# Optimization experiments

Hardware: AMD Instinct MI355X
Metric: run time of the kernel (lower is better)

The kernel has to match this reference:

```python
import jax, jax.numpy as jnp
import numpy as np

NHID = 512
T_K, T_Q, B = 256, 128, 8


def setup_inputs() -> dict:
    key = jax.random.key(0)
    k1, k2, k3, k4, k5 = jax.random.split(key, 5)
    query = jax.random.normal(k1, (T_Q, B, NHID), dtype=jnp.float32)
    c_key = jax.random.normal(k2, (T_K, B, NHID), dtype=jnp.float32)
    mask = jax.random.randint(k3, (T_K, B), 0, 2).astype(bool)
    # att_mlp params: Linear(2*nhid, nhid) -> Tanh -> Linear(nhid, 1)
    # stored as [in, out] so y = x @ W + b (torch Linear weight transposed)
    W1 = jax.random.normal(k4, (2 * NHID, NHID), dtype=jnp.float32) / np.sqrt(2 * NHID)
    b1 = jnp.zeros((NHID,), dtype=jnp.float32)
    W2 = jax.random.normal(k5, (NHID, 1), dtype=jnp.float32) / np.sqrt(NHID)
    b2 = jnp.zeros((1,), dtype=jnp.float32)
    return {"query": query, "c_key": c_key, "mask": mask,
            "W1": W1, "b1": b1, "W2": W2, "b2": b2}


def reference(query, c_key, mask, W1, b1, W2, b2):
    H = query.shape[-1]
    # cat([k_expand, q_expand], -1) @ W1 == k @ W1[:H] + q @ W1[H:]
    # (avoids materializing the [T_k, T_q, B, 2H] concat the torch code builds)
    k_proj = jnp.einsum('kbh,hd->kbd', c_key, W1[:H])   # [T_k, B, H]
    q_proj = jnp.einsum('qbh,hd->qbd', query, W1[H:])   # [T_q, B, H]
    h = jnp.tanh(k_proj[:, None, :, :] + q_proj[None, :, :, :] + b1)  # [T_k, T_q, B, H]
    att_score = jnp.einsum('kqbh,ho->kqb', h, W2) + b2[0]             # [T_k, T_q, B]
    att_score = jnp.where(mask[:, None, :], -jnp.inf, att_score)
    att_prob = jax.nn.softmax(att_score, axis=0)                      # softmax over keys
    # c_val defaults to c_key in the original forward
    ant_vec = jnp.einsum('kqb,kbh->qbh', att_prob, c_key)             # [T_q, B, H]
    return ant_vec, att_prob
```

## Files before the change

### kernel.cpp

```cpp
#include <hip/hip_runtime.h>
#include <math.h>

#define NHID 512
#define T_K  256
#define T_Q  128
#define BB   8

constexpr float C2L2E = 2.8853900817779268f;
constexpr float L2E   = 1.4426950408889634f;

__device__ __forceinline__ float fexp2(float x) { return __builtin_amdgcn_exp2f(x); }
__device__ __forceinline__ float frcp(float x)  { return __builtin_amdgcn_rcpf(x); }

typedef __attribute__((ext_vector_type(8))) short bf16x8;
typedef __attribute__((ext_vector_type(4))) float f32x4;

__device__ __forceinline__ unsigned short f2bf(float x) {
    unsigned u = __builtin_bit_cast(unsigned, x);
    unsigned r = (u + 0x7FFFu + ((u >> 16) & 1u)) >> 16;
    return (unsigned short)r;
}
__device__ __forceinline__ float bf2f(unsigned short h) {
    unsigned u = ((unsigned)h) << 16;
    return __builtin_bit_cast(float, u);
}
__device__ __forceinline__ unsigned packbf(float a, float b) {
    return (unsigned)f2bf(a) | ((unsigned)f2bf(b) << 16);
}

__global__ __launch_bounds__(256) void convert_kernel(
    const float* __restrict__ W1, const float* __restrict__ ckey,
    unsigned short* __restrict__ bt_hi, unsigned short* __restrict__ bt_lo,
    unsigned int* __restrict__ ckp)
{
    const int bid = blockIdx.x;
    const int t   = threadIdx.x;
    if (bid < 128) {
        const int kt = bid & 15;
        const int nt = bid >> 4;
        __shared__ float tile[64][65];
        const int r  = t >> 2;
        const int c0 = (t & 3) * 16;
        const float* src = W1 + (size_t)(kt * 64 + r) * 512 + nt * 64 + c0;
        #pragma unroll
        for (int j = 0; j < 4; ++j) {
            const float4 v = *(const float4*)&src[j * 4];
            tile[r][c0 + j * 4 + 0] = v.x; tile[r][c0 + j * 4 + 1] = v.y;
            tile[r][c0 + j * 4 + 2] = v.z; tile[r][c0 + j * 4 + 3] = v.w;
        }
        __syncthreads();
        const size_t dst = (size_t)((kt >> 3) * 512 + nt * 64 + r) * 512
                         + (size_t)((kt & 7) * 64 + c0);
        #pragma unroll
        for (int j4 = 0; j4 < 4; ++j4) {
            ushort4 h, l;
            #pragma unroll
            for (int e = 0; e < 4; ++e) {
                const float x = tile[c0 + j4 * 4 + e][r];
                const unsigned short hb = f2bf(x);
                ((unsigned short*)&h)[e] = hb;
                ((unsigned short*)&l)[e] = f2bf(x - bf2f(hb));
            }
            *(ushort4*)&bt_hi[dst + j4 * 4] = h;
            *(ushort4*)&bt_lo[dst + j4 * 4] = l;
        }
    } else {
        const int cb = bid - 128;
        const int b  = cb >> 5;
        const int kt = cb & 31;
        const int kloc = t >> 5;
        const int g    = t & 31;
        const int k = kt * 8 + kloc;
        const float* src = ckey + ((size_t)k * 8 + b) * 512 + g * 16;
        const float4 v0 = *(const float4*)&src[0];
        const float4 v1 = *(const float4*)&src[4];
        const float4 v2 = *(const float4*)&src[8];
        const float4 v3 = *(const float4*)&src[12];
        uint4 o0, o1;
        o0.x = packbf(v0.x, v0.y); o0.y = packbf(v0.z, v0.w);
        o0.z = packbf(v1.x, v1.y); o0.w = packbf(v1.z, v1.w);
        o1.x = packbf(v2.x, v2.y); o1.y = packbf(v2.z, v2.w);
        o1.z = packbf(v3.x, v3.y); o1.w = packbf(v3.z, v3.w);
        unsigned int* dst = ckp + ((size_t)b * 256 + k) * 256 + g * 8;
        *(uint4*)&dst[0] = o0;
        *(uint4*)&dst[4] = o1;
    }
}

__global__ __launch_bounds__(256) void proj_kernel(
    const float* __restrict__ qry, const float* __restrict__ ckey,
    const unsigned short* __restrict__ bt_hi, const unsigned short* __restrict__ bt_lo,
    const float* __restrict__ b1,
    uint2* __restrict__ ektq, float* __restrict__ eq)
{
    const int row0 = blockIdx.x * 64;
    const int col0 = blockIdx.y * 64;
    const bool isK = row0 < 2048;
    const int bhalf = isK ? 0 : 512;

    __shared__ __align__(16) unsigned short As_h[64 * 64];
    __shared__ __align__(16) unsigned short As_l[64 * 64];
    __shared__ __align__(16) unsigned short Bs_h[64 * 64];
    __shared__ __align__(16) unsigned short Bs_l[64 * 64];

    const int t    = threadIdx.x;
    const int wave = t >> 6;
    const int lane = t & 63;
    const int wm = (wave & 1) * 32;
    const int wn = (wave >> 1) * 32;

    f32x4 acc[2][2] = {};

    const int sr = t >> 2;
    const int sc = (t & 3) * 16;
    const float* gA = (isK ? ckey + (size_t)(row0 + sr) * 512
                           : qry  + (size_t)(row0 - 2048 + sr) * 512) + sc;
    const unsigned short* gBh = bt_hi + (size_t)(bhalf + col0 + sr) * 512 + sc;
    const unsigned short* gBl = bt_lo + (size_t)(bhalf + col0 + sr) * 512 + sc;
    const int c0c = sc >> 3;
    const int sw0 = ((c0c + 0) ^ (sr & 7)) * 8;
    const int sw1 = ((c0c + 1) ^ (sr & 7)) * 8;

    const int quad = lane >> 4, fr = lane & 15;

    float4 pa0 = *(const float4*)&gA[0];
    float4 pa1 = *(const float4*)&gA[4];
    float4 pa2 = *(const float4*)&gA[8];
    float4 pa3 = *(const float4*)&gA[12];
    uint4  pbh0 = *(const uint4*)&gBh[0], pbh1 = *(const uint4*)&gBh[8];
    uint4  pbl0 = *(const uint4*)&gBl[0], pbl1 = *(const uint4*)&gBl[8];

    for (int k0 = 0; k0 < 512; k0 += 64) {
        float fa[16];
        *(float4*)&fa[0] = pa0; *(float4*)&fa[4] = pa1;
        *(float4*)&fa[8] = pa2; *(float4*)&fa[12] = pa3;
        union { uint4 v; unsigned short s[8]; } h0, l0, h1, l1;
        #pragma unroll
        for (int e = 0; e < 8; ++e) {
            const unsigned short hb = f2bf(fa[e]);
            h0.s[e] = hb; l0.s[e] = f2bf(fa[e] - bf2f(hb));
        }
        #pragma unroll
        for (int e = 0; e < 8; ++e) {
            const unsigned short hb = f2bf(fa[8 + e]);
            h1.s[e] = hb; l1.s[e] = f2bf(fa[8 + e] - bf2f(hb));
        }
        __syncthreads();
        *(uint4*)&As_h[sr * 64 + sw0] = h0.v; *(uint4*)&As_h[sr * 64 + sw1] = h1.v;
        *(uint4*)&As_l[sr * 64 + sw0] = l0.v; *(uint4*)&As_l[sr * 64 + sw1] = l1.v;
        *(uint4*)&Bs_h[sr * 64 + sw0] = pbh0; *(uint4*)&Bs_h[sr * 64 + sw1] = pbh1;
        *(uint4*)&Bs_l[sr * 64 + sw0] = pbl0; *(uint4*)&Bs_l[sr * 64 + sw1] = pbl1;
        __syncthreads();

        if (k0 + 64 < 512) {
            pa0 = *(const float4*)&gA[k0 + 64];
            pa1 = *(const float4*)&gA[k0 + 68];
            pa2 = *(const float4*)&gA[k0 + 72];
            pa3 = *(const float4*)&gA[k0 + 76];
            pbh0 = *(const uint4*)&gBh[k0 + 64]; pbh1 = *(const uint4*)&gBh[k0 + 72];
            pbl0 = *(const uint4*)&gBl[k0 + 64]; pbl1 = *(const uint4*)&gBl[k0 + 72];
        }

        #pragma unroll
        for (int ks = 0; ks < 2; ++ks) {
            const int cchunk = ks * 4 + quad;
            bf16x8 afh[2], afl[2], bfh[2], bfl[2];
            #pragma unroll
            for (int mt = 0; mt < 2; ++mt) {
                const int m = wm + mt * 16 + fr;
                afh[mt] = *(const bf16x8*)&As_h[m * 64 + ((cchunk ^ (m & 7)) * 8)];
                afl[mt] = *(const bf16x8*)&As_l[m * 64 + ((cchunk ^ (m & 7)) * 8)];
            }
            #pragma unroll
            for (int nt = 0; nt < 2; ++nt) {
                const int n = wn + nt * 16 + fr;
                bfh[nt] = *(const bf16x8*)&Bs_h[n * 64 + ((cchunk ^ (n & 7)) * 8)];
                bfl[nt] = *(const bf16x8*)&Bs_l[n * 64 + ((cchunk ^ (n & 7)) * 8)];
            }
            #pragma unroll
            for (int mt = 0; mt < 2; ++mt)
                #pragma unroll
                for (int nt = 0; nt < 2; ++nt) {
                    acc[mt][nt] = __builtin_amdgcn_mfma_f32_16x16x32_bf16(afh[mt], bfh[nt], acc[mt][nt], 0, 0, 0);
                    acc[mt][nt] = __builtin_amdgcn_mfma_f32_16x16x32_bf16(afh[mt], bfl[nt], acc[mt][nt], 0, 0, 0);
                    acc[mt][nt] = __builtin_amdgcn_mfma_f32_16x16x32_bf16(afl[mt], bfh[nt], acc[mt][nt], 0, 0, 0);
                }
        }
    }

    #pragma unroll
    for (int nt = 0; nt < 2; ++nt) {
        const int colg = col0 + wn + nt * 16 + fr;
        const float b1v = b1[colg];
        #pragma unroll
        for (int mt = 0; mt < 2; ++mt) {
            #pragma unroll
            for (int i = 0; i < 4; ++i) {
                const int rowg = row0 + wm + mt * 16 + quad * 4 + i;
                const float v = acc[mt][nt][i];
                if (isK) {
                    const float e = fexp2((v + b1v) * C2L2E);
                    const float ep = __shfl_xor(e, 1, 64);
                    unsigned pk = packbf(e, ep);
                    pk = ((fr & 1) == 0) ? pk
                       : (unsigned)f2bf(ep) | ((unsigned)f2bf(e) << 16);
                    const unsigned pk2 = __shfl_xor(pk, 2, 64);
                    if ((fr & 3) == 0) {
                        const int kidx = rowg >> 3;
                        const int bb   = rowg & 7;
                        const int hq   = colg >> 2;
                        ektq[((size_t)bb * 128 + hq) * 256 + kidx] =
                            make_uint2(pk, pk2);
                    }
                } else {
                    eq[(size_t)(rowg - 2048) * 512 + colg] = fexp2(v * C2L2E);
                }
            }
        }
    }
}

__global__ __launch_bounds__(512) void scoreav_kernel(
    const uint2* __restrict__ ektq, const float* __restrict__ eq,
    const float* __restrict__ W2, const float* __restrict__ b2,
    const int* __restrict__ mask, const unsigned int* __restrict__ ckp,
    float* __restrict__ prob_out, float* __restrict__ out_ant)
{
    const int t    = threadIdx.x;
    const int lane = t & 63;
    const int wave = __builtin_amdgcn_readfirstlane(t >> 6);
    const int kk   = t & 255;
    const int half = t >> 8;
    const int q0   = blockIdx.x * 2;
    const int b    = blockIdx.y;

    __shared__ float eq0s[512], eq1s[512], w2s[512];
    __shared__ float rp[2][512];
    __shared__ float ps[2][256];
    __shared__ float pacc[8][2][512];

    eq0s[t] = eq[((size_t)q0 * 8 + b) * 512 + t];
    eq1s[t] = eq[((size_t)(q0 + 1) * 8 + b) * 512 + t];
    w2s[t]  = W2[t];

    const float4 wA = *(const float4*)&W2[lane * 4];
    const float4 wB = *(const float4*)&W2[256 + lane * 4];
    float s2 = wA.x + wA.y + wA.z + wA.w + wB.x + wB.y + wB.z + wB.w;
    #pragma unroll
    for (int m = 32; m; m >>= 1) s2 += __shfl_xor(s2, m, 64);
    const float base = s2 + b2[0];
    __syncthreads();

    const uint2* __restrict__ ekb = ektq + (size_t)b * 128 * 256 + kk;
    float racc0 = 0.0f, racc1 = 0.0f;

    for (int g = 0; g < 8; ++g) {
        uint2 L[8];
        #pragma unroll
        for (int j = 0; j < 8; ++j)
            L[j] = ekb[(size_t)(half * 64 + g * 8 + j) * 256];
        #pragma unroll
        for (int j = 0; j < 8; ++j) {
            const int h = (half * 64 + g * 8 + j) * 4;
            const float ek0 = __builtin_bit_cast(float, L[j].x << 16);
            const float ek1 = __builtin_bit_cast(float, L[j].x & 0xFFFF0000u);
            const float ek2 = __builtin_bit_cast(float, L[j].y << 16);
            const float ek3 = __builtin_bit_cast(float, L[j].y & 0xFFFF0000u);
            const float4 w  = *(const float4*)&w2s[h];
            const float4 e0 = *(const float4*)&eq0s[h];
            const float4 e1 = *(const float4*)&eq1s[h];
            {
                const float a0 = fmaf(ek0, e0.x, 1.0f);
                const float a1 = fmaf(ek1, e0.y, 1.0f);
                const float a2 = fmaf(ek2, e0.z, 1.0f);
                const float a3 = fmaf(ek3, e0.w, 1.0f);
                const float d01 = a0 * a1, d23 = a2 * a3;
                const float n01 = fmaf(w.x, a1, w.y * a0);
                const float n23 = fmaf(w.z, a3, w.w * a2);
                const float N = fmaf(n01, d23, n23 * d01);
                racc0 = fmaf(N, frcp(d01 * d23), racc0);
            }
            {
                const float a0 = fmaf(ek0, e1.x, 1.0f);
                const float a1 = fmaf(ek1, e1.y, 1.0f);
                const float a2 = fmaf(ek2, e1.z, 1.0f);
                const float a3 = fmaf(ek3, e1.w, 1.0f);
                const float d01 = a0 * a1, d23 = a2 * a3;
                const float n01 = fmaf(w.x, a1, w.y * a0);
                const float n23 = fmaf(w.z, a3, w.w * a2);
                const float N = fmaf(n01, d23, n23 * d01);
                racc1 = fmaf(N, frcp(d01 * d23), racc1);
            }
        }
    }
    rp[0][t] = racc0;
    rp[1][t] = racc1;
    __syncthreads();

    if (t < 256) {
        const int msk = mask[t * 8 + b];
        float s0 = base - 2.0f * (rp[0][t] + rp[0][t + 256]);
        float s1 = base - 2.0f * (rp[1][t] + rp[1][t + 256]);
        if (msk) { s0 = -INFINITY; s1 = -INFINITY; }
        ps[0][t] = s0;
        ps[1][t] = s1;
    }
    __syncthreads();

    if (wave < 2) {
        float4 sv = *(const float4*)&ps[wave][lane * 4];
        float m = fmaxf(fmaxf(sv.x, sv.y), fmaxf(sv.z, sv.w));
        #pragma unroll
        for (int d = 32; d; d >>= 1) m = fmaxf(m, __shfl_xor(m, d, 64));
        float4 pv;
        pv.x = fexp2((sv.x - m) * L2E);
        pv.y = fexp2((sv.y - m) * L2E);
        pv.z = fexp2((sv.z - m) * L2E);
        pv.w = fexp2((sv.w - m) * L2E);
        float sum = pv.x + pv.y + pv.z + pv.w;
        #pragma unroll
        for (int d = 32; d; d >>= 1) sum += __shfl_xor(sum, d, 64);
        const float inv = frcp(sum);
        pv.x *= inv; pv.y *= inv; pv.z *= inv; pv.w *= inv;
        *(float4*)&ps[wave][lane * 4] = pv;
        const int qb_idx = (q0 + wave) * 8 + b;
        const int kbase = lane * 4;
        prob_out[(size_t)(kbase + 0) * 1024 + qb_idx] = pv.x;
        prob_out[(size_t)(kbase + 1) * 1024 + qb_idx] = pv.y;
        prob_out[(size_t)(kbase + 2) * 1024 + qb_idx] = pv.z;
        prob_out[(size_t)(kbase + 3) * 1024 + qb_idx] = pv.w;
    }
    __syncthreads();

    {
        const int h0 = lane * 8;
        float4 aL0 = {}, aH0 = {}, aL1 = {}, aH1 = {};
        const int kstart = wave * 32;
        #pragma unroll 4
        for (int ki = 0; ki < 32; ++ki) {
            const int k = kstart + ki;
            const uint4 U = *(const uint4*)&ckp[((size_t)b * 256 + k) * 256 + lane * 4];
            float4 c0, c1;
            c0.x = __builtin_bit_cast(float, U.x << 16);
            c0.y = __builtin_bit_cast(float, U.x & 0xFFFF0000u);
            c0.z = __builtin_bit_cast(float, U.y << 16);
            c0.w = __builtin_bit_cast(float, U.y & 0xFFFF0000u);
            c1.x = __builtin_bit_cast(float, U.z << 16);
            c1.y = __builtin_bit_cast(float, U.z & 0xFFFF0000u);
            c1.z = __builtin_bit_cast(float, U.w << 16);
            c1.w = __builtin_bit_cast(float, U.w & 0xFFFF0000u);
            const float p0 = ps[0][k];
            const float p1 = ps[1][k];
            aL0.x = fmaf(p0, c0.x, aL0.x); aL0.y = fmaf(p0, c0.y, aL0.y);
            aL0.z = fmaf(p0, c0.z, aL0.z); aL0.w = fmaf(p0, c0.w, aL0.w);
            aH0.x = fmaf(p0, c1.x, aH0.x); aH0.y = fmaf(p0, c1.y, aH0.y);
            aH0.z = fmaf(p0, c1.z, aH0.z); aH0.w = fmaf(p0, c1.w, aH0.w);
            aL1.x = fmaf(p1, c0.x, aL1.x); aL1.y = fmaf(p1, c0.y, aL1.y);
            aL1.z = fmaf(p1, c0.z, aL1.z); aL1.w = fmaf(p1, c0.w, aL1.w);
            aH1.x = fmaf(p1, c1.x, aH1.x); aH1.y = fmaf(p1, c1.y, aH1.y);
            aH1.z = fmaf(p1, c1.z, aH1.z); aH1.w = fmaf(p1, c1.w, aH1.w);
        }
        *(float4*)&pacc[wave][0][h0 + 0] = aL0;
        *(float4*)&pacc[wave][0][h0 + 4] = aH0;
        *(float4*)&pacc[wave][1][h0 + 0] = aL1;
        *(float4*)&pacc[wave][1][h0 + 4] = aH1;
    }
    __syncthreads();

    {
        #pragma unroll
        for (int qi = 0; qi < 2; ++qi) {
            float s = 0.f;
            #pragma unroll
            for (int w = 0; w < 8; ++w) s += pacc[w][qi][t];
            out_ant[((size_t)(q0 + qi) * 8 + b) * 512 + t] = s;
        }
    }
}

extern "C" void kernel_launch(void* const* d_in, const int* in_sizes, int n_in,
                              void* d_out, int out_size, void* d_ws, size_t ws_size,
                              hipStream_t stream)
{
    const float* qry  = (const float*)d_in[0];
    const float* ckey = (const float*)d_in[1];
    const int*   mask = (const int*)d_in[2];
    const float* W1   = (const float*)d_in[3];
    const float* b1   = (const float*)d_in[4];
    const float* W2   = (const float*)d_in[5];
    const float* b2   = (const float*)d_in[6];

    float* out_ant  = (float*)d_out;
    float* out_prob = (float*)d_out + T_Q * BB * NHID;

    float* ws = (float*)d_ws;
    uint2* ws_ektq = (uint2*)ws;
    float* ws_eq  = ws + 524288;
    unsigned short* bt_hi = (unsigned short*)(ws + 1048576);
    unsigned short* bt_lo = (unsigned short*)(ws + 1310720);
    unsigned int* ws_ckp  = (unsigned int*)(ws + 1572864);

    convert_kernel<<<dim3(384), 256, 0, stream>>>(W1, ckey, bt_hi, bt_lo, ws_ckp);
    proj_kernel<<<dim3(48, 8), 256, 0, stream>>>(qry, ckey, bt_hi, bt_lo, b1, ws_ektq, ws_eq);
    scoreav_kernel<<<dim3(64, 8), 512, 0, stream>>>(ws_ektq, ws_eq, W2, b2, mask, ws_ckp,
                                                    out_prob, out_ant);
}
```

Measured before the change: 113.3 us.

## Halve proj_kernel row tile and double-buffer ektq loads in scoreav

The projection GEMM tile shrinks from 64 to 32 rows, doubling the grid from 384 to 768 blocks so more CUs are busy for this small GEMM. Each wave now computes one M-tile instead of two. Separately, the score kernel software-pipelines its loads of the exp(k) data, prefetching the next group of eight rows while the current group is computed. The costs are lower B-tile reuse per block in the GEMM and higher register pressure in the score kernel.

Result: no change. 112.3 us (-0.9%).

```diff
diff --git a/kernel.cpp b/kernel.cpp
--- a/kernel.cpp
+++ b/kernel.cpp
@@ -93,70 +93,64 @@
     const float* __restrict__ b1,
     uint2* __restrict__ ektq, float* __restrict__ eq)
 {
-    const int row0 = blockIdx.x * 64;
+    const int row0 = blockIdx.x * 32;
     const int col0 = blockIdx.y * 64;
     const bool isK = row0 < 2048;
     const int bhalf = isK ? 0 : 512;
 
-    __shared__ __align__(16) unsigned short As_h[64 * 64];
-    __shared__ __align__(16) unsigned short As_l[64 * 64];
+    __shared__ __align__(16) unsigned short As_h[32 * 64];
+    __shared__ __align__(16) unsigned short As_l[32 * 64];
     __shared__ __align__(16) unsigned short Bs_h[64 * 64];
     __shared__ __align__(16) unsigned short Bs_l[64 * 64];
 
     const int t    = threadIdx.x;
     const int wave = t >> 6;
     const int lane = t & 63;
-    const int wm = (wave & 1) * 32;
+    const int wm = (wave & 1) * 16;
     const int wn = (wave >> 1) * 32;
 
-    f32x4 acc[2][2] = {};
-
-    const int sr = t >> 2;
-    const int sc = (t & 3) * 16;
-    const float* gA = (isK ? ckey + (size_t)(row0 + sr) * 512
-                           : qry  + (size_t)(row0 - 2048 + sr) * 512) + sc;
-    const unsigned short* gBh = bt_hi + (size_t)(bhalf + col0 + sr) * 512 + sc;
-    const unsigned short* gBl = bt_lo + (size_t)(bhalf + col0 + sr) * 512 + sc;
-    const int c0c = sc >> 3;
-    const int sw0 = ((c0c + 0) ^ (sr & 7)) * 8;
-    const int sw1 = ((c0c + 1) ^ (sr & 7)) * 8;
+    f32x4 acc[2] = {};
+
+    const int srA = t >> 3;
+    const int scA = (t & 7) * 8;
+    const float* gA = (isK ? ckey + (size_t)(row0 + srA) * 512
+                           : qry  + (size_t)(row0 - 2048 + srA) * 512) + scA;
+    const int swA = ((scA >> 3) ^ (srA & 7)) * 8;
+
+    const int srB = t >> 2;
+    const int scB = (t & 3) * 16;
+    const unsigned short* gBh = bt_hi + (size_t)(bhalf + col0 + srB) * 512 + scB;
+    const unsigned short* gBl = bt_lo + (size_t)(bhalf + col0 + srB) * 512 + scB;
+    const int cB = scB >> 3;
+    const int swB0 = ((cB + 0) ^ (srB & 7)) * 8;
+    const int swB1 = ((cB + 1) ^ (srB & 7)) * 8;
 
     const int quad = lane >> 4, fr = lane & 15;
 
     float4 pa0 = *(const float4*)&gA[0];
     float4 pa1 = *(const float4*)&gA[4];
-    float4 pa2 = *(const float4*)&gA[8];
-    float4 pa3 = *(const float4*)&gA[12];
     uint4  pbh0 = *(const uint4*)&gBh[0], pbh1 = *(const uint4*)&gBh[8];
     uint4  pbl0 = *(const uint4*)&gBl[0], pbl1 = *(const uint4*)&gBl[8];
 
     for (int k0 = 0; k0 < 512; k0 += 64) {
-        float fa[16];
+        float fa[8];
         *(float4*)&fa[0] = pa0; *(float4*)&fa[4] = pa1;
-        *(float4*)&fa[8] = pa2; *(float4*)&fa[12] = pa3;
-        union { uint4 v; unsigned short s[8]; } h0, l0, h1, l1;
+        union { uint4 v; unsigned short s[8]; } h0, l0;
         #pragma unroll
         for (int e = 0; e < 8; ++e) {
             const unsigned short hb = f2bf(fa[e]);
             h0.s[e] = hb; l0.s[e] = f2bf(fa[e] - bf2f(hb));
         }
-        #pragma unroll
-        for (int e = 0; e < 8; ++e) {
-            const unsigned short hb = f2bf(fa[8 + e]);
-            h1.s[e] = hb; l1.s[e] = f2bf(fa[8 + e] - bf2f(hb));
-        }
         __syncthreads();
-        *(uint4*)&As_h[sr * 64 + sw0] = h0.v; *(uint4*)&As_h[sr * 64 + sw1] = h1.v;
-        *(uint4*)&As_l[sr * 64 + sw0] = l0.v; *(uint4*)&As_l[sr * 64 + sw1] = l1.v;
-        *(uint4*)&Bs_h[sr * 64 + sw0] = pbh0; *(uint4*)&Bs_h[sr * 64 + sw1] = pbh1;
-        *(uint4*)&Bs_l[sr * 64 + sw0] = pbl0; *(uint4*)&Bs_l[sr * 64 + sw1] = pbl1;
+        *(uint4*)&As_h[srA * 64 + swA] = h0.v;
+        *(uint4*)&As_l[srA * 64 + swA] = l0.v;
+        *(uint4*)&Bs_h[srB * 64 + swB0] = pbh0; *(uint4*)&Bs_h[srB * 64 + swB1] = pbh1;
+        *(uint4*)&Bs_l[srB * 64 + swB0] = pbl0; *(uint4*)&Bs_l[srB * 64 + swB1] = pbl1;
         __syncthreads();
 
         if (k0 + 64 < 512) {
             pa0 = *(const float4*)&gA[k0 + 64];
             pa1 = *(const float4*)&gA[k0 + 68];
-            pa2 = *(const float4*)&gA[k0 + 72];
-            pa3 = *(const float4*)&gA[k0 + 76];
             pbh0 = *(const uint4*)&gBh[k0 + 64]; pbh1 = *(const uint4*)&gBh[k0 + 72];
             pbl0 = *(const uint4*)&gBl[k0 + 64]; pbl1 = *(const uint4*)&gBl[k0 + 72];
         }
@@ -164,13 +158,10 @@
         #pragma unroll
         for (int ks = 0; ks < 2; ++ks) {
             const int cchunk = ks * 4 + quad;
-            bf16x8 afh[2], afl[2], bfh[2], bfl[2];
-            #pragma unroll
-            for (int mt = 0; mt < 2; ++mt) {
-                const int m = wm + mt * 16 + fr;
-                afh[mt] = *(const bf16x8*)&As_h[m * 64 + ((cchunk ^ (m & 7)) * 8)];
-                afl[mt] = *(const bf16x8*)&As_l[m * 64 + ((cchunk ^ (m & 7)) * 8)];
-            }
+            const int m = wm + fr;
+            const bf16x8 afh = *(const bf16x8*)&As_h[m * 64 + ((cchunk ^ (m & 7)) * 8)];
+            const bf16x8 afl = *(const bf16x8*)&As_l[m * 64 + ((cchunk ^ (m & 7)) * 8)];
+            bf16x8 bfh[2], bfl[2];
             #pragma unroll
             for (int nt = 0; nt < 2; ++nt) {
                 const int n = wn + nt * 16 + fr;
@@ -178,13 +169,11 @@
                 bfl[nt] = *(const bf16x8*)&Bs_l[n * 64 + ((cchunk ^ (n & 7)) * 8)];
             }
             #pragma unroll
-            for (int mt = 0; mt < 2; ++mt)
-                #pragma unroll
-                for (int nt = 0; nt < 2; ++nt) {
-                    acc[mt][nt] = __builtin_amdgcn_mfma_f32_16x16x32_bf16(afh[mt], bfh[nt], acc[mt][nt], 0, 0, 0);
-                    acc[mt][nt] = __builtin_amdgcn_mfma_f32_16x16x32_bf16(afh[mt], bfl[nt], acc[mt][nt], 0, 0, 0);
-                    acc[mt][nt] = __builtin_amdgcn_mfma_f32_16x16x32_bf16(afl[mt], bfh[nt], acc[mt][nt], 0, 0, 0);
-                }
+            for (int nt = 0; nt < 2; ++nt) {
+                acc[nt] = __builtin_amdgcn_mfma_f32_16x16x32_bf16(afh, bfh[nt], acc[nt], 0, 0, 0);
+                acc[nt] = __builtin_amdgcn_mfma_f32_16x16x32_bf16(afh, bfl[nt], acc[nt], 0, 0, 0);
+                acc[nt] = __builtin_amdgcn_mfma_f32_16x16x32_bf16(afl, bfh[nt], acc[nt], 0, 0, 0);
+            }
         }
     }
 
@@ -193,28 +182,22 @@
         const int colg = col0 + wn + nt * 16 + fr;
         const float b1v = b1[colg];
         #pragma unroll
-        for (int mt = 0; mt < 2; ++mt) {
-            #pragma unroll
-            for (int i = 0; i < 4; ++i) {
-                const int rowg = row0 + wm + mt * 16 + quad * 4 + i;
-                const float v = acc[mt][nt][i];
-                if (isK) {
-                    const float e = fexp2((v + b1v) * C2L2E);
-                    const float ep = __shfl_xor(e, 1, 64);
-                    unsigned pk = packbf(e, ep);
-                    pk = ((fr & 1) == 0) ? pk
-                       : (unsigned)f2bf(ep) | ((unsigned)f2bf(e) << 16);
-                    const unsigned pk2 = __shfl_xor(pk, 2, 64);
-                    if ((fr & 3) == 0) {
-                        const int kidx = rowg >> 3;
-                        const int bb   = rowg & 7;
-                        const int hq   = colg >> 2;
-                        ektq[((size_t)bb * 128 + hq) * 256 + kidx] =
-                            make_uint2(pk, pk2);
-                    }
-                } else {
-                    eq[(size_t)(rowg - 2048) * 512 + colg] = fexp2(v * C2L2E);
+        for (int i = 0; i < 4; ++i) {
+            const int rowg = row0 + wm + quad * 4 + i;
+            const float v = acc[nt][i];
+            if (isK) {
+                const float e = fexp2((v + b1v) * C2L2E);
+                const float ep = __shfl_xor(e, 1, 64);
+                unsigned pk = ((fr & 1) == 0) ? packbf(e, ep) : packbf(ep, e);
+                const unsigned pk2 = __shfl_xor(pk, 2, 64);
+                if ((fr & 3) == 0) {
+                    const int kidx = rowg >> 3;
+                    const int bb   = rowg & 7;
+                    const int hq   = colg >> 2;
+                    ektq[((size_t)bb * 128 + hq) * 256 + kidx] = make_uint2(pk, pk2);
                 }
+            } else {
+                eq[(size_t)(rowg - 2048) * 512 + colg] = fexp2(v * C2L2E);
             }
         }
     }
@@ -254,18 +237,25 @@
     const uint2* __restrict__ ekb = ektq + (size_t)b * 128 * 256 + kk;
     float racc0 = 0.0f, racc1 = 0.0f;
 
+    uint2 L[2][8];
+    #pragma unroll
+    for (int j = 0; j < 8; ++j)
+        L[0][j] = ekb[(size_t)(half * 64 + j) * 256];
+
     for (int g = 0; g < 8; ++g) {
-        uint2 L[8];
-        #pragma unroll
-        for (int j = 0; j < 8; ++j)
-            L[j] = ekb[(size_t)(half * 64 + g * 8 + j) * 256];
+        const int cur = g & 1;
+        if (g < 7) {
+            #pragma unroll
+            for (int j = 0; j < 8; ++j)
+                L[cur ^ 1][j] = ekb[(size_t)(half * 64 + (g + 1) * 8 + j) * 256];
+        }
         #pragma unroll
         for (int j = 0; j < 8; ++j) {
             const int h = (half * 64 + g * 8 + j) * 4;
-            const float ek0 = __builtin_bit_cast(float, L[j].x << 16);
-            const float ek1 = __builtin_bit_cast(float, L[j].x & 0xFFFF0000u);
-            const float ek2 = __builtin_bit_cast(float, L[j].y << 16);
-            const float ek3 = __builtin_bit_cast(float, L[j].y & 0xFFFF0000u);
+            const float ek0 = __builtin_bit_cast(float, L[cur][j].x << 16);
+            const float ek1 = __builtin_bit_cast(float, L[cur][j].x & 0xFFFF0000u);
+            const float ek2 = __builtin_bit_cast(float, L[cur][j].y << 16);
+            const float ek3 = __builtin_bit_cast(float, L[cur][j].y & 0xFFFF0000u);
             const float4 w  = *(const float4*)&w2s[h];
             const float4 e0 = *(const float4*)&eq0s[h];
             const float4 e1 = *(const float4*)&eq1s[h];
@@ -401,7 +391,7 @@
     unsigned int* ws_ckp  = (unsigned int*)(ws + 1572864);
 
     convert_kernel<<<dim3(384), 256, 0, stream>>>(W1, ckey, bt_hi, bt_lo, ws_ckp);
-    proj_kernel<<<dim3(48, 8), 256, 0, stream>>>(qry, ckey, bt_hi, bt_lo, b1, ws_ektq, ws_eq);
+    proj_kernel<<<dim3(96, 8), 256, 0, stream>>>(qry, ckey, bt_hi, bt_lo, b1, ws_ektq, ws_eq);
     scoreav_kernel<<<dim3(64, 8), 512, 0, stream>>>(ws_ektq, ws_eq, W2, b2, mask, ws_ckp,
                                                     out_prob, out_ant);
 }
```
